# Kernel optimization log

Hardware: AMD Instinct MI355X
Metric: run time of the kernel (lower is better)

Reference implementation:

```python
import jax, jax.numpy as jnp
import numpy as np

N_ENT = 40000      # n_ent_vocab
NUM_POS = 24       # n_rel_vocab // 2
N_REL = 48         # n_rel_vocab (fwd + inverse relations)
BODY_LEN = 3
N_EDGES = 300000
BATCH = 64
THR = 1e-20


def setup_inputs() -> dict:
    key = jax.random.key(0)
    ks = jax.random.split(key, 8)
    return {
        "q_head": jax.random.randint(ks[0], (BATCH,), 0, N_ENT, dtype=jnp.int32),
        "q_rel": jax.random.randint(ks[1], (BATCH,), 0, NUM_POS, dtype=jnp.int32),
        "t": jax.random.randint(ks[2], (BATCH,), 0, N_ENT, dtype=jnp.int32),
        # dec_output is a softmax over relations -> positive weights in (0,1)
        "attention": jax.random.uniform(ks[3], (BATCH, BODY_LEN, N_REL), dtype=jnp.float32),
        "edge_head": jax.random.randint(ks[4], (N_EDGES,), 0, N_ENT, dtype=jnp.int32),
        "edge_tail": jax.random.randint(ks[5], (N_EDGES,), 0, N_ENT, dtype=jnp.int32),
        "edge_rel": jax.random.randint(ks[6], (N_EDGES,), 0, NUM_POS, dtype=jnp.int32),
        # uncertain-KG confidence values stored in the sparse adjacency
        "edge_val": jax.random.uniform(ks[7], (N_EDGES,), dtype=jnp.float32),
    }


def reference(q_head, q_rel, t, attention, edge_head, edge_tail, edge_rel, edge_val):
    """Fused equivalent of Translator.forwardAllNLP.

    database[r] are sparse [N_ENT, N_ENT] matrices; here the whole multigraph is
    one edge list (edge_head, edge_tail, edge_rel, edge_val). torch.sparse.mm
    per relation + attention-weighted accumulation becomes a single gather /
    segment_sum pass over all relations at once.
    """
    B = q_head.shape[0]
    # zero out the query triples in the (shared) database, as in the torch code
    killed = ((edge_head[None, :] == q_head[:, None])
              & (edge_tail[None, :] == t[:, None])
              & (edge_rel[None, :] == q_rel[:, None])).any(axis=0)
    vals = jnp.where(killed, 0.0, edge_val)  # [E]

    mem = jax.nn.one_hot(q_head, N_ENT, dtype=jnp.float32)  # [B, N_ENT]
    for step in range(BODY_LEN):
        attn = attention[:, step]                 # [B, N_REL]
        a_fwd = attn[:, edge_rel]                 # [B, E]  attention[:,step,r]
        a_rev = attn[:, edge_rel + NUM_POS]       # [B, E]  attention[:,step,r+num_pos]
        gh = mem[:, edge_head] * vals             # [B, E]  sparse.mm(mem, A_r)
        gt = mem[:, edge_tail] * vals             # [B, E]  sparse.mm(mem, A_r^T)
        fwd_msg = jax.ops.segment_sum((gh * a_fwd).T, edge_tail, num_segments=N_ENT).T
        rev_msg = jax.ops.segment_sum((gt * a_rev).T, edge_head, num_segments=N_ENT).T
        # self-loop term: memories * attention[:, step, -1]
        mem = fwd_msg + rev_msg + mem * attn[:, -1:]

    mem = mem / jnp.maximum(THR, mem.sum(axis=1, keepdims=True))
    # -sum(one_hot(t) * log(max(thr, mem))) == -log(max(thr, mem[b, t[b]]))
    tgt_prob = mem[jnp.arange(B), t]
    batch_loss = -jnp.log(jnp.maximum(THR, tgt_prob)).mean()
    return batch_loss, mem
```

## Files before the change

kernel.cpp:

```cpp
#include <hip/hip_runtime.h>

#define N_ENT 40000
#define NB 64
#define BODY_LEN 3
#define N_REL 48
#define NUM_POS 24
#define THR 1e-20f

#define NBK 313
#define PA_BLOCKS 320
#define DEC_BLOCKS 320
#define FLIST_LDS 192


__global__ void k_build0(const int* __restrict__ eh, const int* __restrict__ et,
                         int* __restrict__ pHist, const int* __restrict__ qh,
                         const float* __restrict__ attn, float* __restrict__ memA,
                         int* __restrict__ fcnt, int* __restrict__ flist,
                         float* __restrict__ sums, int nE) {
    int tid = threadIdx.x;
    if (blockIdx.x < PA_BLOCKS) {
        __shared__ int h[NBK];
        for (int i = tid; i < NBK; i += 256) h[i] = 0;
        __syncthreads();
        int chunk = (nE + PA_BLOCKS - 1) / PA_BLOCKS;
        int b0 = blockIdx.x * chunk, b1 = min(nE, b0 + chunk);
        for (int i = b0 + tid; i < b1; i += 256) {
            atomicAdd(&h[eh[i] >> 7], 1);
            atomicAdd(&h[et[i] >> 7], 1);
        }
        __syncthreads();
        for (int i = tid; i < NBK; i += 256) pHist[blockIdx.x * NBK + i] = h[i];
    } else {
        __shared__ float s_d[NB];
        __shared__ int s_q[NB];
        if (tid < NB) {
            s_d[tid] = attn[tid * (BODY_LEN * N_REL) + 0 * N_REL + (N_REL - 1)];
            s_q[tid] = qh[tid];
        }
        __syncthreads();
        int ib = blockIdx.x - PA_BLOCKS;
        const int total4 = NB * N_ENT / 4;
        for (int i4 = ib * 256 + tid; i4 < total4; i4 += 320 * 256) {
            int ent = (i4 * 4) >> 6;
            int b0 = (i4 * 4) & 63;
            float4 w;
            w.x = (s_q[b0 + 0] == ent) ? s_d[b0 + 0] : 0.0f;
            w.y = (s_q[b0 + 1] == ent) ? s_d[b0 + 1] : 0.0f;
            w.z = (s_q[b0 + 2] == ent) ? s_d[b0 + 2] : 0.0f;
            w.w = (s_q[b0 + 3] == ent) ? s_d[b0 + 3] : 0.0f;
            ((float4*)memA)[i4] = w;
        }
        if (ib == 0) {
            for (int i = tid; i < NB * 16; i += 256) sums[i] = 0.0f;
            if (tid < 64) {
                int q = s_q[tid];
                bool first = true;
                for (int j = 0; j < tid; ++j) first &= (s_q[j] != q);
                unsigned long long mf = __ballot(first);
                int pos = __popcll(mf & ((1ULL << tid) - 1ULL));
                if (first) flist[pos] = q;
                if (tid == 0) fcnt[0] = __popcll(mf);
                if (tid == 1) fcnt[1] = 0;
                if (tid == 2) fcnt[2] = 0;
            }
        }
    }
}

__global__ void k_bcol(int* __restrict__ pHist, int* __restrict__ bktTot) {
    __shared__ int s[512];
    int t = threadIdx.x, b = blockIdx.x;
    int v = (t < PA_BLOCKS) ? pHist[t * NBK + b] : 0;
    s[t] = v;
    __syncthreads();
    for (int off = 1; off < 512; off <<= 1) {
        int add = (t >= off) ? s[t - off] : 0;
        __syncthreads();
        s[t] += add;
        __syncthreads();
    }
    if (t < PA_BLOCKS) pHist[t * NBK + b] = s[t] - v;
    if (t == PA_BLOCKS - 1) bktTot[b] = s[t];
}

__global__ void k_bscan_small(const int* __restrict__ bktTot, int* __restrict__ bktBase,
                              int* __restrict__ offs) {
    __shared__ int s[512];
    int t = threadIdx.x;
    int v = (t < NBK) ? bktTot[t] : 0;
    s[t] = v;
    __syncthreads();
    for (int off = 1; off < 512; off <<= 1) {
        int add = (t >= off) ? s[t - off] : 0;
        __syncthreads();
        s[t] += add;
        __syncthreads();
    }
    if (t < NBK) bktBase[t] = s[t] - v;
    if (t == NBK - 1) { bktBase[NBK] = s[t]; offs[N_ENT] = s[t]; }
}

__global__ void k_passA(const int* __restrict__ qh, const int* __restrict__ qr,
                        const int* __restrict__ tq, const int* __restrict__ eh,
                        const int* __restrict__ et, const int* __restrict__ er,
                        const float* __restrict__ ev, const int* __restrict__ pBase,
                        const int* __restrict__ bktBase, uint2* __restrict__ items, int nE) {
    __shared__ long long s_key[NB];
    __shared__ int cur[NBK];
    int tid = threadIdx.x;
    if (tid < NB)
        s_key[tid] = ((long long)qh[tid] << 32) | ((long long)tq[tid] << 8) | (long long)qr[tid];
    for (int i = tid; i < NBK; i += 256)
        cur[i] = bktBase[i] + pBase[blockIdx.x * NBK + i];
    __syncthreads();
    int chunk = (nE + PA_BLOCKS - 1) / PA_BLOCKS;
    int b0 = blockIdx.x * chunk, b1 = min(nE, b0 + chunk);
    for (int i = b0 + tid; i < b1; i += 256) {
        int hh = eh[i], te = et[i], r = er[i];
        long long k = ((long long)hh << 32) | ((long long)te << 8) | (long long)r;
        bool killed = false;
#pragma unroll
        for (int b = 0; b < NB; ++b) killed |= (s_key[b] == k);
        unsigned vb = killed ? 0u : __float_as_uint(ev[i]);
        int bk = hh >> 7;
        int p = atomicAdd(&cur[bk], 1);
        items[p] = make_uint2((unsigned)te | ((unsigned)r << 16) |
                              ((unsigned)(hh & 127) << 24), vb);
        bk = te >> 7;
        p = atomicAdd(&cur[bk], 1);
        items[p] = make_uint2((unsigned)hh | ((unsigned)(r + NUM_POS) << 16) |
                              ((unsigned)(te & 127) << 24), vb);
    }
}

__global__ void k_passB(const uint2* __restrict__ itemsA, const int* __restrict__ bktBase,
                        int* __restrict__ offs, uint2* __restrict__ csr) {
    __shared__ int cnt[128];
    __shared__ int sc[256];
    int tid = threadIdx.x;
    int b = blockIdx.x;
    int e0 = b << 7;
    int eCnt = min(128, N_ENT - e0);
    if (tid < 128) cnt[tid] = 0;
    __syncthreads();
    int ib = bktBase[b];
    int n = bktBase[b + 1] - ib;
    for (int i = tid; i < n; i += 256)
        atomicAdd(&cnt[itemsA[ib + i].x >> 24], 1);
    __syncthreads();
    int v = (tid < 128) ? cnt[tid] : 0;
    sc[tid] = v;
    __syncthreads();
    for (int off = 1; off < 256; off <<= 1) {
        int add = (tid >= off) ? sc[tid - off] : 0;
        __syncthreads();
        sc[tid] += add;
        __syncthreads();
    }
    int ex = sc[tid] - v;
    if (tid < eCnt) offs[e0 + tid] = ib + ex;
    if (tid < 128) cnt[tid] = ex;
    __syncthreads();
    for (int i = tid; i < n; i += 256) {
        uint2 it = itemsA[ib + i];
        int k = (int)(it.x >> 24);
        int p = atomicAdd(&cnt[k], 1);
        csr[ib + p] = it;
    }
}

__device__ __forceinline__ void flag_entities(unsigned long long m, int lane,
                                              int ent, int* s_cnt, int* s_list) {
    bool flag = ((lane & 15) == 0) && ((m >> lane) & 0xFFFFULL);
    unsigned long long am = __ballot(flag);
    if (am) {
        int leader = __ffsll((long long)am) - 1;
        int lb = 0;
        if (lane == leader) lb = atomicAdd(s_cnt, __popcll(am));
        lb = __shfl(lb, leader);
        if (flag) {
            int rank = __popcll(am & ((1ULL << lane) - 1ULL));
            s_list[lb + rank] = ent;
        }
    }
}

__global__ void k_decay(const float* __restrict__ oldm, float* __restrict__ nxt,
                        const float* __restrict__ attn, int step,
                        int* __restrict__ fcnt, int* __restrict__ flist,
                        float* __restrict__ sums) {
    __shared__ float s_d[NB];
    __shared__ float s_s[NB];
    __shared__ int s_list[FLIST_LDS];
    __shared__ int s_cnt, s_gbase;
    int tid = threadIdx.x;
    if (tid < NB) {
        s_d[tid] = attn[tid * (BODY_LEN * N_REL) + step * N_REL + (N_REL - 1)];
        s_s[tid] = 0.0f;
    }
    if (tid == 0) s_cnt = 0;
    __syncthreads();
    int lane = tid & 63;
    int b0 = (tid * 4) & 63;
    float cs0 = 0.0f, cs1 = 0.0f, cs2 = 0.0f, cs3 = 0.0f;
    const int total4 = NB * N_ENT / 4;
    for (int i4 = blockIdx.x * 256 + tid; i4 < total4; i4 += gridDim.x * 256) {
        float4 v = ((const float4*)oldm)[i4];
        float4 w;
        w.x = v.x * s_d[b0 + 0];
        w.y = v.y * s_d[b0 + 1];
        w.z = v.z * s_d[b0 + 2];
        w.w = v.w * s_d[b0 + 3];
        ((float4*)nxt)[i4] = w;
        if (sums) { cs0 += w.x; cs1 += w.y; cs2 += w.z; cs3 += w.w; }
        bool nz = (v.x != 0.0f) | (v.y != 0.0f) | (v.z != 0.0f) | (v.w != 0.0f);
        unsigned long long m = __ballot(nz);
        flag_entities(m, lane, (i4 * 4) >> 6, &s_cnt, s_list);
    }
    __syncthreads();
    if (tid == 0 && s_cnt) s_gbase = atomicAdd(fcnt, s_cnt);
    __syncthreads();
    for (int i = tid; i < s_cnt; i += 256) flist[s_gbase + i] = s_list[i];
    if (sums) {
        atomicAdd(&s_s[b0 + 0], cs0);
        atomicAdd(&s_s[b0 + 1], cs1);
        atomicAdd(&s_s[b0 + 2], cs2);
        atomicAdd(&s_s[b0 + 3], cs3);
        __syncthreads();
        if (tid < NB) atomicAdd(&sums[tid * 16], s_s[tid]);
    }
}

template <bool STEP0>
__global__ __launch_bounds__(256) void k_fstep(
    const uint2* __restrict__ csr, const int* __restrict__ offs,
    const int* __restrict__ flist, const int* __restrict__ fcnt,
    const float* __restrict__ attn, int step,
    const float* __restrict__ oldm, const int* __restrict__ qh,
    float* __restrict__ nxt, float* __restrict__ sums) {
    __shared__ float s_attn[NB][N_REL + 1];
    __shared__ float s_s[NB];
    int tid = threadIdx.x;
    for (int idx = tid; idx < NB * N_REL; idx += 256) {
        int b = idx / N_REL, r = idx % N_REL;
        s_attn[b][r] = attn[b * (BODY_LEN * N_REL) + step * N_REL + r];
    }
    if (tid < NB) s_s[tid] = 0.0f;
    __syncthreads();
    int lane = tid & 63;
    int myqh = STEP0 ? qh[lane] : 0;
    float colsum = 0.0f;
    int n = *fcnt;
    int w = (blockIdx.x * 256 + tid) >> 6;
    int nW = (gridDim.x * 256) >> 6;
    for (int f = w; f < n; f += nW) {
        int e = flist[f];
        float src = STEP0 ? ((myqh == e) ? 1.0f : 0.0f)
                          : oldm[(size_t)e * 64 + lane];
        int base = offs[e];
        int cnt = offs[e + 1] - base;
        for (int k0 = 0; k0 < cnt; k0 += 64) {
            uint2 slot = make_uint2(0u, 0u);
            if (k0 + lane < cnt) slot = csr[base + k0 + lane];
            int lim = min(64, cnt - k0);
            for (int j = 0; j < lim; ++j) {
                unsigned meta = (unsigned)__shfl((int)slot.x, j);
                float v = __uint_as_float((unsigned)__shfl((int)slot.y, j));
                if (v == 0.0f) continue;
                float val = src * v * s_attn[lane][(meta >> 16) & 63];
                if (val != 0.0f) {
                    atomicAdd(&nxt[(size_t)(meta & 0xFFFFu) * 64 + lane], val);
                    if (sums) colsum += val;
                }
            }
        }
    }
    if (sums) {
        atomicAdd(&s_s[lane], colsum);
        __syncthreads();
        if (tid < NB) atomicAdd(&sums[tid * 16], s_s[tid]);
    }
}

__global__ void k_norm_tr(const float* __restrict__ mem, const float* __restrict__ sums,
                          const int* __restrict__ tt, float* __restrict__ out) {
    if (blockIdx.x == N_ENT / 64) {
        int b = threadIdx.x;
        if (b < 64) {
            float p = mem[(size_t)tt[b] * 64 + b] / fmaxf(THR, sums[b * 16]);
            float l = -logf(fmaxf(THR, p));
#pragma unroll
            for (int off = 32; off > 0; off >>= 1) l += __shfl_down(l, off);
            if (b == 0) out[0] = l * (1.0f / 64.0f);
        }
        return;
    }
    __shared__ float tile[64][65];
    __shared__ float s_inv[64];
    int tid = threadIdx.x;
    int e0 = blockIdx.x * 64;
    if (tid < 64) s_inv[tid] = 1.0f / fmaxf(THR, sums[tid * 16]);
    const float4* m4 = (const float4*)(mem + (size_t)e0 * 64);
#pragma unroll
    for (int k = 0; k < 4; ++k) {
        int i4 = k * 256 + tid;
        float4 v = m4[i4];
        int el = i4 >> 4, b0 = (i4 * 4) & 63;
        tile[el][b0 + 0] = v.x; tile[el][b0 + 1] = v.y;
        tile[el][b0 + 2] = v.z; tile[el][b0 + 3] = v.w;
    }
    __syncthreads();
#pragma unroll
    for (int k = 0; k < 16; ++k) {
        int idx = k * 256 + tid;
        int el = idx & 63, b = idx >> 6;
        out[1 + (size_t)b * N_ENT + e0 + el] = tile[el][b] * s_inv[b];
    }
}

extern "C" void kernel_launch(void* const* d_in, const int* in_sizes, int n_in,
                              void* d_out, int out_size, void* d_ws, size_t ws_size,
                              hipStream_t stream) {
    const int*   qh   = (const int*)d_in[0];
    const int*   qr   = (const int*)d_in[1];
    const int*   tt   = (const int*)d_in[2];
    const float* attn = (const float*)d_in[3];
    const int*   eh   = (const int*)d_in[4];
    const int*   et   = (const int*)d_in[5];
    const int*   er   = (const int*)d_in[6];
    const float* ev   = (const float*)d_in[7];
    float* out = (float*)d_out;
    int nE = in_sizes[4];

    const size_t MEM_BYTES = (size_t)NB * N_ENT * sizeof(float);
    char* ws = (char*)d_ws;
    int*   offs    = (int*)ws;
    int*   flist   = (int*)(ws + (192u << 10));
    int*   pHist   = (int*)(ws + (384u << 10));
    int*   bktTot  = (int*)(ws + (896u << 10));
    int*   bktBase = (int*)(ws + (900u << 10));
    int*   fcnt    = (int*)(ws + (904u << 10));
    float* sums    = (float*)(ws + (908u << 10));
    uint2* csr     = (uint2*)(ws + (1u << 20));
    float* memA    = (float*)(ws + (6u << 20));
    float* memB;
    uint2* itemsA;
    size_t itemsBytes = (size_t)2 * nE * sizeof(uint2);
    size_t needBoth = (size_t)(6u << 20) + 2 * MEM_BYTES + itemsBytes;
    if (ws_size >= needBoth) {
        memB   = (float*)(ws + (6u << 20) + MEM_BYTES);
        itemsA = (uint2*)(ws + (6u << 20) + 2 * MEM_BYTES);
    } else {
        memB   = out + 1;
        itemsA = (uint2*)(out + 1);
    }

    k_build0<<<2 * PA_BLOCKS, 256, 0, stream>>>(eh, et, pHist, qh, attn, memA,
                                                fcnt, flist, sums, nE);
    k_bcol<<<NBK, 512, 0, stream>>>(pHist, bktTot);
    k_bscan_small<<<1, 512, 0, stream>>>(bktTot, bktBase, offs);
    k_passA<<<PA_BLOCKS, 256, 0, stream>>>(qh, qr, tt, eh, et, er, ev, pHist,
                                           bktBase, itemsA, nE);
    k_passB<<<NBK, 256, 0, stream>>>(itemsA, bktBase, offs, csr);

    k_fstep<true><<<16, 256, 0, stream>>>(csr, offs, flist, fcnt + 0, attn, 0,
                                          nullptr, qh, memA, nullptr);
    k_decay<<<DEC_BLOCKS, 256, 0, stream>>>(memA, memB, attn, 1, fcnt + 1, flist, nullptr);
    k_fstep<false><<<1024, 256, 0, stream>>>(csr, offs, flist, fcnt + 1, attn, 1,
                                             memA, nullptr, memB, nullptr);
    k_decay<<<DEC_BLOCKS, 256, 0, stream>>>(memB, memA, attn, 2, fcnt + 2, flist, sums);
    k_fstep<false><<<1024, 256, 0, stream>>>(csr, offs, flist, fcnt + 2, attn, 2,
                                             memB, nullptr, memA, sums);

    k_norm_tr<<<N_ENT / 64 + 1, 256, 0, stream>>>(memA, sums, tt, out);
}
```

Measured before the change: 210.0 us.

## Precompute CSR ranges in frontier list and stage edges via LDS with unrolled scatter

The frontier list entries become int4 records carrying the entity, its CSR offset and its edge count, filled in by the decay kernel, so the propagation kernel skips the dependent offs lookups. The propagation inner loop now stages each 64-edge chunk in LDS and processes four edges per iteration instead of broadcasting every edge with two shuffles. Blocks with no frontier work exit early. Grid sizes for init, decay and propagation are raised. In exchange the frontier list takes more memory traffic, the workspace layout is shifted, and the larger grids add launch and scheduling cost.

```diff
diff --git a/kernel.cpp b/kernel.cpp
--- a/kernel.cpp
+++ b/kernel.cpp
@@ -9,14 +9,16 @@
 
 #define NBK 313
 #define PA_BLOCKS 320
-#define DEC_BLOCKS 320
+#define INIT_BLOCKS 960
+#define DEC_BLOCKS 1280
+#define FSTEP_BLOCKS 2048
 #define FLIST_LDS 192
 
 
 __global__ void k_build0(const int* __restrict__ eh, const int* __restrict__ et,
                          int* __restrict__ pHist, const int* __restrict__ qh,
                          const float* __restrict__ attn, float* __restrict__ memA,
-                         int* __restrict__ fcnt, int* __restrict__ flist,
+                         int* __restrict__ fcnt, int4* __restrict__ flist,
                          float* __restrict__ sums, int nE) {
     int tid = threadIdx.x;
     if (blockIdx.x < PA_BLOCKS) {
@@ -41,7 +43,7 @@
         __syncthreads();
         int ib = blockIdx.x - PA_BLOCKS;
         const int total4 = NB * N_ENT / 4;
-        for (int i4 = ib * 256 + tid; i4 < total4; i4 += 320 * 256) {
+        for (int i4 = ib * 256 + tid; i4 < total4; i4 += INIT_BLOCKS * 256) {
             int ent = (i4 * 4) >> 6;
             int b0 = (i4 * 4) & 63;
             float4 w;
@@ -59,7 +61,7 @@
                 for (int j = 0; j < tid; ++j) first &= (s_q[j] != q);
                 unsigned long long mf = __ballot(first);
                 int pos = __popcll(mf & ((1ULL << tid) - 1ULL));
-                if (first) flist[pos] = q;
+                if (first) flist[pos] = make_int4(q, 0, 0, 0);
                 if (tid == 0) fcnt[0] = __popcll(mf);
                 if (tid == 1) fcnt[1] = 0;
                 if (tid == 2) fcnt[2] = 0;
@@ -188,7 +190,8 @@
 
 __global__ void k_decay(const float* __restrict__ oldm, float* __restrict__ nxt,
                         const float* __restrict__ attn, int step,
-                        int* __restrict__ fcnt, int* __restrict__ flist,
+                        const int* __restrict__ offs,
+                        int* __restrict__ fcnt, int4* __restrict__ flist,
                         float* __restrict__ sums) {
     __shared__ float s_d[NB];
     __shared__ float s_s[NB];
@@ -221,7 +224,12 @@
     __syncthreads();
     if (tid == 0 && s_cnt) s_gbase = atomicAdd(fcnt, s_cnt);
     __syncthreads();
-    for (int i = tid; i < s_cnt; i += 256) flist[s_gbase + i] = s_list[i];
+    for (int i = tid; i < s_cnt; i += 256) {
+        int e = s_list[i];
+        int base = offs[e];
+        int c = offs[e + 1] - base;
+        flist[s_gbase + i] = make_int4(e, base, c, 0);
+    }
     if (sums) {
         atomicAdd(&s_s[b0 + 0], cs0);
         atomicAdd(&s_s[b0 + 1], cs1);
@@ -235,44 +243,57 @@
 template <bool STEP0>
 __global__ __launch_bounds__(256) void k_fstep(
     const uint2* __restrict__ csr, const int* __restrict__ offs,
-    const int* __restrict__ flist, const int* __restrict__ fcnt,
+    const int4* __restrict__ flist, const int* __restrict__ fcnt,
     const float* __restrict__ attn, int step,
     const float* __restrict__ oldm, const int* __restrict__ qh,
     float* __restrict__ nxt, float* __restrict__ sums) {
     __shared__ float s_attn[NB][N_REL + 1];
     __shared__ float s_s[NB];
-    int tid = threadIdx.x;
+    __shared__ uint2 s_it[4][64];
+    int tid = threadIdx.x;
+    int n = *fcnt;
+    if ((int)(blockIdx.x * 4) >= n) return;
     for (int idx = tid; idx < NB * N_REL; idx += 256) {
         int b = idx / N_REL, r = idx % N_REL;
         s_attn[b][r] = attn[b * (BODY_LEN * N_REL) + step * N_REL + r];
     }
     if (tid < NB) s_s[tid] = 0.0f;
     __syncthreads();
-    int lane = tid & 63;
+    int lane = tid & 63, wv = tid >> 6;
     int myqh = STEP0 ? qh[lane] : 0;
     float colsum = 0.0f;
-    int n = *fcnt;
     int w = (blockIdx.x * 256 + tid) >> 6;
     int nW = (gridDim.x * 256) >> 6;
     for (int f = w; f < n; f += nW) {
-        int e = flist[f];
+        int4 fe = flist[f];
+        int e = fe.x;
+        int base, cnt;
+        if (STEP0) { base = offs[e]; cnt = offs[e + 1] - base; }
+        else       { base = fe.y;    cnt = fe.z; }
         float src = STEP0 ? ((myqh == e) ? 1.0f : 0.0f)
                           : oldm[(size_t)e * 64 + lane];
-        int base = offs[e];
-        int cnt = offs[e + 1] - base;
         for (int k0 = 0; k0 < cnt; k0 += 64) {
-            uint2 slot = make_uint2(0u, 0u);
-            if (k0 + lane < cnt) slot = csr[base + k0 + lane];
             int lim = min(64, cnt - k0);
-            for (int j = 0; j < lim; ++j) {
-                unsigned meta = (unsigned)__shfl((int)slot.x, j);
-                float v = __uint_as_float((unsigned)__shfl((int)slot.y, j));
-                if (v == 0.0f) continue;
-                float val = src * v * s_attn[lane][(meta >> 16) & 63];
-                if (val != 0.0f) {
-                    atomicAdd(&nxt[(size_t)(meta & 0xFFFFu) * 64 + lane], val);
-                    if (sums) colsum += val;
-                }
+            if (lane < lim) s_it[wv][lane] = csr[base + k0 + lane];
+            int j = 0;
+            for (; j + 4 <= lim; j += 4) {
+                uint2 a0 = s_it[wv][j + 0], a1 = s_it[wv][j + 1];
+                uint2 a2 = s_it[wv][j + 2], a3 = s_it[wv][j + 3];
+                float t0 = src * __uint_as_float(a0.y) * s_attn[lane][(a0.x >> 16) & 63];
+                float t1 = src * __uint_as_float(a1.y) * s_attn[lane][(a1.x >> 16) & 63];
+                float t2 = src * __uint_as_float(a2.y) * s_attn[lane][(a2.x >> 16) & 63];
+                float t3 = src * __uint_as_float(a3.y) * s_attn[lane][(a3.x >> 16) & 63];
+                if (t0 != 0.0f) atomicAdd(&nxt[(size_t)(a0.x & 0xFFFFu) * 64 + lane], t0);
+                if (t1 != 0.0f) atomicAdd(&nxt[(size_t)(a1.x & 0xFFFFu) * 64 + lane], t1);
+                if (t2 != 0.0f) atomicAdd(&nxt[(size_t)(a2.x & 0xFFFFu) * 64 + lane], t2);
+                if (t3 != 0.0f) atomicAdd(&nxt[(size_t)(a3.x & 0xFFFFu) * 64 + lane], t3);
+                colsum += t0 + t1 + t2 + t3;
+            }
+            for (; j < lim; ++j) {
+                uint2 a0 = s_it[wv][j];
+                float t0 = src * __uint_as_float(a0.y) * s_attn[lane][(a0.x >> 16) & 63];
+                if (t0 != 0.0f) atomicAdd(&nxt[(size_t)(a0.x & 0xFFFFu) * 64 + lane], t0);
+                colsum += t0;
             }
         }
     }
@@ -336,28 +357,28 @@
     const size_t MEM_BYTES = (size_t)NB * N_ENT * sizeof(float);
     char* ws = (char*)d_ws;
     int*   offs    = (int*)ws;
-    int*   flist   = (int*)(ws + (192u << 10));
-    int*   pHist   = (int*)(ws + (384u << 10));
-    int*   bktTot  = (int*)(ws + (896u << 10));
-    int*   bktBase = (int*)(ws + (900u << 10));
-    int*   fcnt    = (int*)(ws + (904u << 10));
-    float* sums    = (float*)(ws + (908u << 10));
-    uint2* csr     = (uint2*)(ws + (1u << 20));
-    float* memA    = (float*)(ws + (6u << 20));
+    int*   pHist   = (int*)(ws + (192u << 10));
+    int*   bktTot  = (int*)(ws + (592u << 10));
+    int*   bktBase = (int*)(ws + (596u << 10));
+    int*   fcnt    = (int*)(ws + (600u << 10));
+    float* sums    = (float*)(ws + (604u << 10));
+    int4*  flist   = (int4*)(ws + (640u << 10));
+    uint2* csr     = (uint2*)(ws + (2u << 20));
+    float* memA    = (float*)(ws + (7u << 20));
     float* memB;
     uint2* itemsA;
     size_t itemsBytes = (size_t)2 * nE * sizeof(uint2);
-    size_t needBoth = (size_t)(6u << 20) + 2 * MEM_BYTES + itemsBytes;
+    size_t needBoth = (size_t)(7u << 20) + 2 * MEM_BYTES + itemsBytes;
     if (ws_size >= needBoth) {
-        memB   = (float*)(ws + (6u << 20) + MEM_BYTES);
-        itemsA = (uint2*)(ws + (6u << 20) + 2 * MEM_BYTES);
+        memB   = (float*)(ws + (7u << 20) + MEM_BYTES);
+        itemsA = (uint2*)(ws + (7u << 20) + 2 * MEM_BYTES);
     } else {
         memB   = out + 1;
         itemsA = (uint2*)(out + 1);
     }
 
-    k_build0<<<2 * PA_BLOCKS, 256, 0, stream>>>(eh, et, pHist, qh, attn, memA,
-                                                fcnt, flist, sums, nE);
+    k_build0<<<PA_BLOCKS + INIT_BLOCKS, 256, 0, stream>>>(eh, et, pHist, qh, attn, memA,
+                                                          fcnt, flist, sums, nE);
     k_bcol<<<NBK, 512, 0, stream>>>(pHist, bktTot);
     k_bscan_small<<<1, 512, 0, stream>>>(bktTot, bktBase, offs);
     k_passA<<<PA_BLOCKS, 256, 0, stream>>>(qh, qr, tt, eh, et, er, ev, pHist,
@@ -366,12 +387,14 @@
 
     k_fstep<true><<<16, 256, 0, stream>>>(csr, offs, flist, fcnt + 0, attn, 0,
                                           nullptr, qh, memA, nullptr);
-    k_decay<<<DEC_BLOCKS, 256, 0, stream>>>(memA, memB, attn, 1, fcnt + 1, flist, nullptr);
-    k_fstep<false><<<1024, 256, 0, stream>>>(csr, offs, flist, fcnt + 1, attn, 1,
-                                             memA, nullptr, memB, nullptr);
-    k_decay<<<DEC_BLOCKS, 256, 0, stream>>>(memB, memA, attn, 2, fcnt + 2, flist, sums);
-    k_fstep<false><<<1024, 256, 0, stream>>>(csr, offs, flist, fcnt + 2, attn, 2,
-                                             memB, nullptr, memA, sums);
+    k_decay<<<DEC_BLOCKS, 256, 0, stream>>>(memA, memB, attn, 1, offs,
+                                            fcnt + 1, flist, nullptr);
+    k_fstep<false><<<FSTEP_BLOCKS, 256, 0, stream>>>(csr, offs, flist, fcnt + 1, attn, 1,
+                                                     memA, nullptr, memB, nullptr);
+    k_decay<<<DEC_BLOCKS, 256, 0, stream>>>(memB, memA, attn, 2, offs,
+                                            fcnt + 2, flist, sums);
+    k_fstep<false><<<FSTEP_BLOCKS, 256, 0, stream>>>(csr, offs, flist, fcnt + 2, attn, 2,
+                                                     memB, nullptr, memA, sums);
 
     k_norm_tr<<<N_ENT / 64 + 1, 256, 0, stream>>>(memA, sums, tt, out);
 }
```

Result: slower. 258.9 us (+23.3%).
